# Optimization experiments

Hardware: AMD Instinct MI355X
Metric: run time of the kernel (lower is better)

The kernel has to match this reference:

```python
import jax, jax.numpy as jnp
import numpy as np

K = 16          # num clusters
DZ = 64         # dim_zt == dim_zi (required by decoder matmul)
DT = 1024       # treatment feature dim (dim_t)
NT = 2048       # number of treatments == dim_x (columns of input_ins)
NI = 4096       # number of instances
MU_P_WT = 5.0
COS_EPS = 1e-6


def setup_inputs() -> dict:
    key = jax.random.key(0)
    ks = jax.random.split(key, 12)
    s = 0.02
    return {
        "input_ins": jax.random.uniform(ks[0], (NI, NT), dtype=jnp.float32),
        "input_treat": jax.random.normal(ks[1], (NT, DT), dtype=jnp.float32),
        # nn.Linear params (torch layout: W [out, in], y = x @ W.T + b)
        "W_mu_zt": jax.random.normal(ks[2], (DZ, DT)) * s,
        "b_mu_zt": jnp.zeros((DZ,), jnp.float32),
        "W_lv_zt": jax.random.normal(ks[3], (DZ, DT)) * s,
        "b_lv_zt": jnp.zeros((DZ,), jnp.float32),
        "W_arec": jax.random.normal(ks[4], (DT, DZ)) * s,
        "b_arec": jnp.zeros((DT,), jnp.float32),
        "W_mu_zi": jax.random.normal(ks[5], (DZ, NT)) * s,
        "b_mu_zi": jnp.zeros((DZ,), jnp.float32),
        "W_lv_zi": jax.random.normal(ks[6], (DZ, NT)) * s,
        "b_lv_zi": jnp.zeros((DZ,), jnp.float32),
        "mu_p_zt": jax.random.normal(ks[7], (K, DZ), dtype=jnp.float32),
        "logvar_p_zt": jnp.ones((K, DZ), jnp.float32),
        "W_y1": jax.random.normal(ks[8], (K * DZ, DZ)) * s,
        "b_y1": jnp.zeros((K * DZ,), jnp.float32),
        "W_y2": jax.random.normal(ks[9], (1, K * DZ)) * s,
        "b_y2": jnp.zeros((1,), jnp.float32),
    }


def reference(input_ins, input_treat, W_mu_zt, b_mu_zt, W_lv_zt, b_lv_zt,
              W_arec, b_arec, W_mu_zi, b_mu_zi, W_lv_zi, b_lv_zi,
              mu_p_zt, logvar_p_zt, W_y1, b_y1, W_y2, b_y2):
    # encode_t (eval mode: zt_sample = mu_zt)
    mu_zt = input_treat @ W_mu_zt.T + b_mu_zt           # [NT, DZ]
    logvar_zt = input_treat @ W_lv_zt.T + b_lv_zt       # [NT, DZ]
    zt = mu_zt

    # compute_qc (cosine similarity vs scaled cluster centers, *10)
    centers = MU_P_WT * mu_p_zt                          # [K, DZ]
    num = zt @ centers.T                                 # [NT, K]
    denom = jnp.maximum(
        jnp.linalg.norm(zt, axis=1, keepdims=True) * jnp.linalg.norm(centers, axis=1)[None, :],
        COS_EPS)
    qc_raw = 10.0 * num / denom                          # [NT, K]
    cates = jax.nn.softmax(qc_raw, axis=1)               # forward softmaxes qc once
    c_sample = jax.nn.softmax(cates, axis=1)             # encode_i (eval) softmaxes again

    # encode_i, vectorized over K clusters: (input_ins * cates_k) @ W.T + b
    # fused einsum avoids materializing the [K, NI, NT] masked inputs
    mu_zi = jnp.einsum('nt,tk,dt->knd', input_ins, c_sample, W_mu_zi) + b_mu_zi       # [K, NI, DZ]
    logvar_zi = jnp.einsum('nt,tk,dt->knd', input_ins, c_sample, W_lv_zi) + b_lv_zi   # [K, NI, DZ]
    zi = mu_zi  # eval-mode reparameterize

    # a_reconstby_zt
    a_reconst = jax.nn.sigmoid(zt @ W_arec.T + b_arec)   # [NT, DT]

    # decoder: sum_k sigmoid(zi_k @ zt.T) * cates_k
    logits = jnp.einsum('knd,td->knt', zi, zt)           # [K, NI, NT]
    a_pred = jnp.einsum('knt,tk->nt', jax.nn.sigmoid(logits), c_sample)  # [NI, NT]

    # predictY
    zi_all = jnp.transpose(zi, (1, 0, 2)).reshape(zi.shape[1], K * DZ)   # cat over k, dim=1
    a_zt = input_ins @ zt                                # [NI, DZ]
    rep_w1 = a_zt @ W_y1.T + b_y1                        # [NI, K*DZ]
    pred_y2 = zi_all @ W_y2.T + b_y2                     # [NI, 1]
    # diag(rep_w1 @ zi_all.T) == rowwise dot product (no NIxNI matmul)
    mu_y = jnp.sum(rep_w1 * zi_all, axis=1, keepdims=True) + pred_y2     # [NI, 1]
    logvar_y = jnp.ones_like(mu_y)

    return (mu_zt, logvar_zt, mu_p_zt, logvar_p_zt, cates, mu_zi, logvar_zi,
            zi, a_pred, mu_y, logvar_y, a_reconst)
```

## Files before the change

### kernel.cpp

```cpp
#include <hip/hip_runtime.h>

typedef unsigned short ushort_t;
typedef unsigned int   uint32;
typedef __attribute__((ext_vector_type(8))) short short8;
typedef __attribute__((ext_vector_type(4))) float f32x4;

#define DEV __device__ __forceinline__

#define KC 16
#define DZ 64
#define DT 1024
#define NT 2048
#define NI 4096
#define KD 1024

#define O_MU_ZT   0
#define O_LV_ZT   131072
#define O_MU_P    262144
#define O_LV_P    263168
#define O_CATES   264192
#define O_MU_ZI   296960
#define O_LV_ZI   4491264
#define O_ZI      8685568
#define O_APRED   12879872
#define O_MU_Y    21268480
#define O_LV_Y    21272576
#define O_AREC    21276672

#define WSF_ZT   0
#define WSF_C    131072
#define WSF_CT   163840
#define WSF_AZT  196608
#define WSF_END  458752
#define WSU_ZTB  0
#define WSU_BC   131072
#define WSU_ZIB  4325376
#define WSU_INSB 8519680
#define WSU_ZHT  16908288
#define WSU_ZLT  17039360

DEV ushort_t f2b(float f){
  uint32 u = __float_as_uint(f);
  u += 0x7fffu + ((u >> 16) & 1u);
  return (ushort_t)(u >> 16);
}
DEV uint32 pk(float lo, float hi){
  return (__float_as_uint(hi) & 0xffff0000u) | (__float_as_uint(lo) >> 16);
}
DEV float wred64(float v){
#pragma unroll
  for (int m = 32; m; m >>= 1) v += __shfl_xor(v, m, 64);
  return v;
}
DEV float fastrcp(float x){ return __builtin_amdgcn_rcpf(x); }
DEV void gl2lds16(ushort_t* l, const ushort_t* g){
  __builtin_amdgcn_global_load_lds(
      (const __attribute__((address_space(1))) unsigned int*)g,
      (__attribute__((address_space(3))) unsigned int*)l, 16, 0, 0);
}

__global__ __launch_bounds__(256) void k_encode_t(
    const float* __restrict__ treat, const float* __restrict__ Wmu,
    const float* __restrict__ bmu, const float* __restrict__ Wlv,
    const float* __restrict__ blv, float* __restrict__ out,
    float* __restrict__ ws_zt)
{
  __shared__ float rowsh[8 * DT];
  const int n0 = blockIdx.x * 8, tid = threadIdx.x;
  const float4* src = (const float4*)(treat + (size_t)n0 * DT);
#pragma unroll
  for (int i = 0; i < 8; ++i)
    ((float4*)rowsh)[tid + i * 256] = src[tid + i * 256];
  __syncthreads();
  const int j = tid & 127, half = tid >> 7;
  const bool isMu = j < 64;
  const int jj = j & 63;
  const float* W = (isMu ? Wmu : Wlv) + (size_t)jj * DT;
  const float bias = isMu ? bmu[jj] : blv[jj];
  float a0 = bias, a1 = bias, a2 = bias, a3 = bias;
  const float4* w4 = (const float4*)W;
  const float4* r0 = (const float4*)&rowsh[(half*4 + 0) * DT];
  const float4* r1 = (const float4*)&rowsh[(half*4 + 1) * DT];
  const float4* r2 = (const float4*)&rowsh[(half*4 + 2) * DT];
  const float4* r3 = (const float4*)&rowsh[(half*4 + 3) * DT];
#pragma unroll 4
  for (int i = 0; i < DT / 4; ++i){
    float4 wv = w4[i];
    float4 v0 = r0[i], v1 = r1[i], v2 = r2[i], v3 = r3[i];
    a0 += wv.x*v0.x + wv.y*v0.y + wv.z*v0.z + wv.w*v0.w;
    a1 += wv.x*v1.x + wv.y*v1.y + wv.z*v1.z + wv.w*v1.w;
    a2 += wv.x*v2.x + wv.y*v2.y + wv.z*v2.z + wv.w*v2.w;
    a3 += wv.x*v3.x + wv.y*v3.y + wv.z*v3.z + wv.w*v3.w;
  }
  float acc[4] = {a0, a1, a2, a3};
#pragma unroll
  for (int r = 0; r < 4; ++r){
    const int row = n0 + half*4 + r;
    if (isMu){ out[O_MU_ZT + row*DZ + jj] = acc[r]; ws_zt[row*DZ + jj] = acc[r]; }
    else     { out[O_LV_ZT + row*DZ + jj] = acc[r]; }
  }
}

__global__ __launch_bounds__(256) void k_qc(
    const float* __restrict__ mu_p, const float* __restrict__ ws_zt,
    float* __restrict__ out, float* __restrict__ ws_c, float* __restrict__ ws_cT)
{
  const int tid = threadIdx.x, lane = tid & 63;
  const int row = blockIdx.x * 4 + (tid >> 6);
  const float z = ws_zt[row * DZ + lane];
  const float nz = sqrtf(wred64(z * z));
  float myqc = 0.f;
#pragma unroll
  for (int k = 0; k < KC; ++k){
    float cv  = 5.f * mu_p[k * DZ + lane];
    float dot = wred64(z * cv);
    float nc2 = wred64(cv * cv);
    float qc  = 10.f * dot / fmaxf(nz * sqrtf(nc2), 1e-6f);
    if (lane == k) myqc = qc;
  }
  float mx = myqc;
#pragma unroll
  for (int m = 8; m; m >>= 1) mx = fmaxf(mx, __shfl_xor(mx, m, 16));
  float e = __expf(myqc - mx);
  float s = e;
#pragma unroll
  for (int m = 8; m; m >>= 1) s += __shfl_xor(s, m, 16);
  float cates = e / s;
  float mx2 = cates;
#pragma unroll
  for (int m = 8; m; m >>= 1) mx2 = fmaxf(mx2, __shfl_xor(mx2, m, 16));
  float e2 = __expf(cates - mx2);
  float s2 = e2;
#pragma unroll
  for (int m = 8; m; m >>= 1) s2 += __shfl_xor(s2, m, 16);
  float c2 = e2 / s2;
  if (lane < KC){
    out[O_CATES + row * KC + lane] = cates;
    ws_c[row * KC + lane] = c2;
    ws_cT[lane * NT + row] = c2;
  }
}

__global__ __launch_bounds__(256) void k_prep(
    const float* __restrict__ Wmu, const float* __restrict__ Wlv,
    const float* __restrict__ cT, const float* __restrict__ zt,
    const float* __restrict__ ins,
    ushort_t* __restrict__ Bc, ushort_t* __restrict__ ztb,
    ushort_t* __restrict__ insb,
    ushort_t* __restrict__ zhT, ushort_t* __restrict__ zlT,
    const float* __restrict__ mu_p, const float* __restrict__ lv_p,
    float* __restrict__ out)
{
  const int bx = blockIdx.x, tid = threadIdx.x;
  if (bx < 2048){
    const int j = bx;
    const bool isMu = j < KD;
    const int kk = (j & (KD-1)) >> 6, d = j & 63;
    const float* W = (isMu ? Wmu : Wlv) + (size_t)d * NT;
    const float* c = cT + (size_t)kk * NT;
    const int t = tid * 8;
    float4 w0 = *(const float4*)(W + t), w1 = *(const float4*)(W + t + 4);
    float4 c0 = *(const float4*)(c + t), c1 = *(const float4*)(c + t + 4);
    ushort_t v[8];
    v[0]=f2b(w0.x*c0.x); v[1]=f2b(w0.y*c0.y); v[2]=f2b(w0.z*c0.z); v[3]=f2b(w0.w*c0.w);
    v[4]=f2b(w1.x*c1.x); v[5]=f2b(w1.y*c1.y); v[6]=f2b(w1.z*c1.z); v[7]=f2b(w1.w*c1.w);
    *(uint4*)(Bc + (size_t)j * NT + t) = *(uint4*)v;
  } else if (bx < 2080){
    const int g = (bx - 2048) * 256 + tid;
    const int base = g * 16;
    const float4* src = (const float4*)(zt + base);
    float4 z0 = src[0], z1 = src[1], z2 = src[2], z3 = src[3];
    ushort_t v[16];
    v[0]=f2b(z0.x); v[1]=f2b(z0.y); v[2]=f2b(z0.z); v[3]=f2b(z0.w);
    v[4]=f2b(z1.x); v[5]=f2b(z1.y); v[6]=f2b(z1.z); v[7]=f2b(z1.w);
    v[8]=f2b(z2.x); v[9]=f2b(z2.y); v[10]=f2b(z2.z); v[11]=f2b(z2.w);
    v[12]=f2b(z3.x); v[13]=f2b(z3.y); v[14]=f2b(z3.z); v[15]=f2b(z3.w);
    *(uint4*)(ztb + base) = *(uint4*)&v[0];
    *(uint4*)(ztb + base + 8) = *(uint4*)&v[8];
  } else if (bx < 2084){
    const int i = (bx - 2080) * 256 + tid;
    out[O_MU_P + i] = mu_p[i];
    out[O_LV_P + i] = lv_p[i];
  } else if (bx < 4132){
    const int g = (bx - 2084) * 256 + tid;
    const int base = g * 16;
    const float4* src = (const float4*)(ins + base);
    float4 z0 = src[0], z1 = src[1], z2 = src[2], z3 = src[3];
    ushort_t v[16];
    v[0]=f2b(z0.x); v[1]=f2b(z0.y); v[2]=f2b(z0.z); v[3]=f2b(z0.w);
    v[4]=f2b(z1.x); v[5]=f2b(z1.y); v[6]=f2b(z1.z); v[7]=f2b(z1.w);
    v[8]=f2b(z2.x); v[9]=f2b(z2.y); v[10]=f2b(z2.z); v[11]=f2b(z2.w);
    v[12]=f2b(z3.x); v[13]=f2b(z3.y); v[14]=f2b(z3.z); v[15]=f2b(z3.w);
    *(uint4*)(insb + base) = *(uint4*)&v[0];
    *(uint4*)(insb + base + 8) = *(uint4*)&v[8];
  } else {
    __shared__ float zsh[64 * 65];
    const int t0 = (bx - 4132) * 64;
#pragma unroll
    for (int jj = 0; jj < 16; ++jj){
      const int idx = jj * 256 + tid;
      const int t = idx >> 6, d = idx & 63;
      zsh[t * 65 + d] = zt[(size_t)(t0 + t) * DZ + d];
    }
    __syncthreads();
    const int d = tid >> 2, tq = tid & 3;
    ushort_t vh[16], vl[16];
#pragma unroll
    for (int i = 0; i < 16; ++i){
      const float f = zsh[(tq * 16 + i) * 65 + d];
      const uint32 u = __float_as_uint(f);
      vh[i] = (ushort_t)(u >> 16);
      const float hf = __uint_as_float(u & 0xffff0000u);
      vl[i] = (ushort_t)(__float_as_uint(f - hf) >> 16);
    }
    *(uint4*)(zhT + (size_t)d * NT + t0 + tq * 16)     = *(uint4*)&vh[0];
    *(uint4*)(zhT + (size_t)d * NT + t0 + tq * 16 + 8) = *(uint4*)&vh[8];
    *(uint4*)(zlT + (size_t)d * NT + t0 + tq * 16)     = *(uint4*)&vl[0];
    *(uint4*)(zlT + (size_t)d * NT + t0 + tq * 16 + 8) = *(uint4*)&vl[8];
  }
}

__global__ __launch_bounds__(256) void k_encode_i(
    const ushort_t* __restrict__ insb, const ushort_t* __restrict__ Bc,
    const float* __restrict__ bmu, const float* __restrict__ blv,
    float* __restrict__ out, ushort_t* __restrict__ zib)
{
  __shared__ ushort_t As[2*128*64];
  __shared__ ushort_t Bs[2*128*64];
  const int tid = threadIdx.x;
  const int orig = blockIdx.y * 16 + blockIdx.x;
  const int swz  = (orig & 7) * 64 + (orig >> 3);
  const int j0 = (swz & 15) * 128, n0 = (swz >> 4) * 128;
  const int w = tid >> 6, lane = tid & 63;
  const int wm = w & 1, wn = w >> 1;
  const int l16 = lane & 15, quad = lane >> 4;

  const int srow = tid >> 3, schunk = (tid & 7) ^ (srow & 7);
  const ushort_t* aSrc = insb + (size_t)(n0 + srow) * NT + schunk * 8;
  const ushort_t* bSrc = Bc  + (size_t)(j0 + srow) * NT + schunk * 8;

  f32x4 acc[4][4] = {};

#pragma unroll
  for (int i = 0; i < 4; ++i){
    gl2lds16(&As[tid*8] + i * 2048, aSrc + (size_t)i * 32 * NT);
    gl2lds16(&Bs[tid*8] + i * 2048, bSrc + (size_t)i * 32 * NT);
  }
  __syncthreads();

  int cur = 0;
  for (int kt = 0; kt < NT/64; ++kt){
    if (kt < NT/64 - 1){
      const ushort_t* ak = aSrc + (kt+1) * 64;
      const ushort_t* bk = bSrc + (kt+1) * 64;
      ushort_t* ad = &As[(cur^1)*8192 + tid*8];
      ushort_t* bd = &Bs[(cur^1)*8192 + tid*8];
#pragma unroll
      for (int i = 0; i < 4; ++i){
        gl2lds16(ad + i * 2048, ak + (size_t)i * 32 * NT);
        gl2lds16(bd + i * 2048, bk + (size_t)i * 32 * NT);
      }
    }
    const ushort_t* Ab = &As[cur*8192];
    const ushort_t* Bb = &Bs[cur*8192];
#pragma unroll
    for (int ks = 0; ks < 2; ++ks){
      const int rsw = ((ks*4 + quad) ^ (l16 & 7)) * 8;
      short8 af[4], bf[4];
#pragma unroll
      for (int mf = 0; mf < 4; ++mf)
        af[mf] = *(const short8*)&Ab[(wm*64 + mf*16 + l16)*64 + rsw];
#pragma unroll
      for (int nf = 0; nf < 4; ++nf)
        bf[nf] = *(const short8*)&Bb[(wn*64 + nf*16 + l16)*64 + rsw];
      __builtin_amdgcn_s_setprio(1);
#pragma unroll
      for (int mf = 0; mf < 4; ++mf)
#pragma unroll
        for (int nf = 0; nf < 4; ++nf)
          acc[mf][nf] = __builtin_amdgcn_mfma_f32_16x16x32_bf16(af[mf], bf[nf], acc[mf][nf], 0, 0, 0);
      __builtin_amdgcn_s_setprio(0);
    }
    __syncthreads();
    cur ^= 1;
  }

  const int colW = j0 + wn * 64;
  const bool isMu = colW < KD;
  const int kk = (colW & (KD - 1)) >> 6;
  const float* bias = isMu ? bmu : blv;
  const size_t zbase = (size_t)kk * (NI * DZ);
#pragma unroll
  for (int mf = 0; mf < 4; ++mf){
    const int r = n0 + wm*64 + mf*16 + quad*4;
#pragma unroll
    for (int nf = 0; nf < 4; ++nf){
      const int d = nf*16 + l16;
      const float bv = bias[d];
#pragma unroll
      for (int reg = 0; reg < 4; ++reg){
        float v = acc[mf][nf][reg] + bv;
        size_t idx = zbase + (size_t)(r + reg)*DZ + d;
        if (isMu){
          out[O_MU_ZI + idx] = v;
          out[O_ZI + idx] = v;
          zib[idx] = f2b(v);
        } else {
          out[O_LV_ZI + idx] = v;
        }
      }
    }
  }
}

__global__ __launch_bounds__(256) void k_decoder(
    const ushort_t* __restrict__ ztb, const ushort_t* __restrict__ zib,
    const float* __restrict__ ws_c, float* __restrict__ out)
{
  __shared__ ushort_t Zt[64*64];
  __shared__ ushort_t Zi[128*64];
  __shared__ float ct[64*17];
  const int tid = threadIdx.x;
  const int t0 = blockIdx.x * 64, n0 = blockIdx.y * 128;
  const int w = tid >> 6, lane = tid & 63;
  const int wm = w & 1, wn = w >> 1;
  const int l16 = lane & 15, quad = lane >> 4;
  const int zr = tid >> 2, zq = tid & 3;
  const int ir = tid >> 1, ih = tid & 1;
  {
    const uint4* src = (const uint4*)(ztb + (size_t)(t0 + zr)*DZ + zq*16);
    uint4 z0 = src[0], z1 = src[1];
    ushort_t* dst = &Zt[zr*64];
    *(uint4*)&dst[((zq*2 + 0) ^ (zr & 7)) * 8] = z0;
    *(uint4*)&dst[((zq*2 + 1) ^ (zr & 7)) * 8] = z1;
  }
  for (int i = tid; i < 64*16; i += 256){
    int t = i >> 4, k = i & 15;
    ct[t*17 + k] = ws_c[(size_t)(t0 + t)*KC + k];
  }
  __syncthreads();
  short8 bfh[2][2];
#pragma unroll
  for (int ks = 0; ks < 2; ++ks){
    const int rsw = ((ks*4 + quad) ^ (l16 & 7)) * 8;
#pragma unroll
    for (int nf = 0; nf < 2; ++nf)
      bfh[ks][nf] = *(const short8*)&Zt[(wn*32 + nf*16 + l16)*64 + rsw];
  }
  const ushort_t* iG = zib + (size_t)(n0 + ir)*DZ + ih*32;
  ushort_t* isw = &Zi[ir*64];
  const int sw0 = ((ih*4 + 0) ^ (ir & 7)) * 8;
  const int sw1 = ((ih*4 + 1) ^ (ir & 7)) * 8;
  const int sw2 = ((ih*4 + 2) ^ (ir & 7)) * 8;
  const int sw3 = ((ih*4 + 3) ^ (ir & 7)) * 8;
  uint4 Zr0, Zr1, Zr2, Zr3;
  {
    const uint4* zp = (const uint4*)iG;
    Zr0 = zp[0]; Zr1 = zp[1]; Zr2 = zp[2]; Zr3 = zp[3];
  }
  f32x4 accum[4][2] = {};
  for (int k = 0; k < KC; ++k){
    __syncthreads();
    *(uint4*)&isw[sw0] = Zr0; *(uint4*)&isw[sw1] = Zr1;
    *(uint4*)&isw[sw2] = Zr2; *(uint4*)&isw[sw3] = Zr3;
    __syncthreads();
    if (k < KC - 1){
      const uint4* zp = (const uint4*)(iG + (size_t)(k+1)*(NI*DZ));
      Zr0 = zp[0]; Zr1 = zp[1]; Zr2 = zp[2]; Zr3 = zp[3];
    }
    f32x4 s[4][2] = {};
#pragma unroll
    for (int ks = 0; ks < 2; ++ks){
      const int rsw = ((ks*4 + quad) ^ (l16 & 7)) * 8;
      short8 af[4];
#pragma unroll
      for (int mf = 0; mf < 4; ++mf)
        af[mf] = *(const short8*)&Zi[(wm*64 + mf*16 + l16)*64 + rsw];
#pragma unroll
      for (int mf = 0; mf < 4; ++mf)
#pragma unroll
        for (int nf = 0; nf < 2; ++nf)
          s[mf][nf] = __builtin_amdgcn_mfma_f32_16x16x32_bf16(af[mf], bfh[ks][nf], s[mf][nf], 0, 0, 0);
    }
#pragma unroll
    for (int nf = 0; nf < 2; ++nf){
      const float cv = ct[(wn*32 + nf*16 + l16)*17 + k];
#pragma unroll
      for (int mf = 0; mf < 4; ++mf)
#pragma unroll
        for (int reg = 0; reg < 4; ++reg)
          accum[mf][nf][reg] += cv * fastrcp(1.f + __expf(-s[mf][nf][reg]));
    }
  }
#pragma unroll
  for (int mf = 0; mf < 4; ++mf){
    const int r = n0 + wm*64 + mf*16 + quad*4;
#pragma unroll
    for (int nf = 0; nf < 2; ++nf){
      const int col = t0 + wn*32 + nf*16 + l16;
#pragma unroll
      for (int reg = 0; reg < 4; ++reg)
        out[O_APRED + (size_t)(r + reg)*NT + col] = accum[mf][nf][reg];
    }
  }
}

__global__ __launch_bounds__(512) void k_arec(
    const float* __restrict__ ws_zt, const float* __restrict__ W,
    const float* __restrict__ bias, float* __restrict__ out)
{
  __shared__ float zsh[8 * DZ];
  const int n0 = blockIdx.x * 8, tid = threadIdx.x;
  if (tid < 128)
    ((float4*)zsh)[tid] = ((const float4*)(ws_zt + (size_t)n0 * DZ))[tid];
  __syncthreads();
#pragma unroll
  for (int jo = 0; jo < 2; ++jo){
    const int j = jo*512 + tid;
    const float4* w4 = (const float4*)(W + (size_t)j * DZ);
    const float b = bias[j];
    float acc[8];
#pragma unroll
    for (int r = 0; r < 8; ++r) acc[r] = b;
#pragma unroll
    for (int i = 0; i < 16; ++i){
      float4 wv = w4[i];
#pragma unroll
      for (int r = 0; r < 8; ++r){
        const float* z = &zsh[r*DZ + i*4];
        acc[r] += wv.x*z[0] + wv.y*z[1] + wv.z*z[2] + wv.w*z[3];
      }
    }
#pragma unroll
    for (int r = 0; r < 8; ++r)
      out[O_AREC + (size_t)(n0 + r)*DT + j] = fastrcp(1.f + __expf(-acc[r]));
  }
}

__global__ __launch_bounds__(512) void k_azt(
    const float* __restrict__ ins, const ushort_t* __restrict__ zhT,
    const ushort_t* __restrict__ zlT, float* __restrict__ azt)
{
  __shared__ float red[16*64];
  const int tid = threadIdx.x;
  const int n0 = blockIdx.x * 16;
  const int w = tid >> 6, lane = tid & 63;
  const int kh = w >> 2, wd = w & 3;
  const int l16 = lane & 15, quad = lane >> 4;
  const float* aRow = ins + (size_t)(n0 + l16) * NT + kh * 1024 + quad * 8;
  const ushort_t* bh = zhT + (size_t)(wd * 16 + l16) * NT + kh * 1024 + quad * 8;
  const ushort_t* bl = zlT + (size_t)(wd * 16 + l16) * NT + kh * 1024 + quad * 8;
  f32x4 acc = {};
#pragma unroll 4
  for (int kt = 0; kt < 16; ++kt){
#pragma unroll
    for (int ks = 0; ks < 2; ++ks){
      const int ko = kt * 64 + ks * 32;
      float4 a0 = *(const float4*)(aRow + ko);
      float4 a1 = *(const float4*)(aRow + ko + 4);
      uint32 u0 = __float_as_uint(a0.x), u1 = __float_as_uint(a0.y);
      uint32 u2 = __float_as_uint(a0.z), u3 = __float_as_uint(a0.w);
      uint32 u4 = __float_as_uint(a1.x), u5 = __float_as_uint(a1.y);
      uint32 u6 = __float_as_uint(a1.z), u7 = __float_as_uint(a1.w);
      uint4 H, L;
      H.x = (u1 & 0xffff0000u) | (u0 >> 16);
      H.y = (u3 & 0xffff0000u) | (u2 >> 16);
      H.z = (u5 & 0xffff0000u) | (u4 >> 16);
      H.w = (u7 & 0xffff0000u) | (u6 >> 16);
      float l0 = a0.x - __uint_as_float(u0 & 0xffff0000u);
      float l1 = a0.y - __uint_as_float(u1 & 0xffff0000u);
      float l2 = a0.z - __uint_as_float(u2 & 0xffff0000u);
      float l3 = a0.w - __uint_as_float(u3 & 0xffff0000u);
      float l4 = a1.x - __uint_as_float(u4 & 0xffff0000u);
      float l5 = a1.y - __uint_as_float(u5 & 0xffff0000u);
      float l6 = a1.z - __uint_as_float(u6 & 0xffff0000u);
      float l7 = a1.w - __uint_as_float(u7 & 0xffff0000u);
      L.x = pk(l0, l1); L.y = pk(l2, l3); L.z = pk(l4, l5); L.w = pk(l6, l7);
      short8 ah = *(short8*)&H, al = *(short8*)&L;
      short8 bh8 = *(const short8*)(bh + ko);
      short8 bl8 = *(const short8*)(bl + ko);
      acc = __builtin_amdgcn_mfma_f32_16x16x32_bf16(ah, bh8, acc, 0, 0, 0);
      acc = __builtin_amdgcn_mfma_f32_16x16x32_bf16(al, bh8, acc, 0, 0, 0);
      acc = __builtin_amdgcn_mfma_f32_16x16x32_bf16(ah, bl8, acc, 0, 0, 0);
    }
  }
  const int col = wd * 16 + l16;
  if (kh == 1){
#pragma unroll
    for (int reg = 0; reg < 4; ++reg)
      red[(quad*4 + reg)*64 + col] = acc[reg];
  }
  __syncthreads();
  if (kh == 0){
#pragma unroll
    for (int reg = 0; reg < 4; ++reg)
      azt[(size_t)(n0 + quad*4 + reg) * DZ + col] = acc[reg] + red[(quad*4 + reg)*64 + col];
  }
}

__global__ __launch_bounds__(512) void k_muy(
    const float* __restrict__ azt, const float* __restrict__ Wy1,
    const float* __restrict__ by1, const float* __restrict__ Wy2,
    const float* __restrict__ by2, const float* __restrict__ zi_out,
    float* __restrict__ out)
{
  __shared__ float sazt[16][DZ];
  const int tid = threadIdx.x;
  const int n0 = blockIdx.x * 16;
  for (int i = tid; i < 16*DZ; i += 512)
    sazt[i >> 6][i & 63] = azt[(size_t)(n0 + (i >> 6))*DZ + (i & 63)];
  __syncthreads();
  const int w = tid >> 6, lane = tid & 63;
  float s0 = 0.f, s1 = 0.f;
  for (int jj = 0; jj < 16; ++jj){
    const int j = jj*64 + lane;
    const float4* wr = (const float4*)(Wy1 + (size_t)j * DZ);
    float d0 = 0.f, d1 = 0.f;
    const float* a0 = sazt[w*2 + 0];
    const float* a1 = sazt[w*2 + 1];
#pragma unroll
    for (int i = 0; i < 16; ++i){
      float4 wv = wr[i];
      d0 += wv.x*a0[i*4] + wv.y*a0[i*4+1] + wv.z*a0[i*4+2] + wv.w*a0[i*4+3];
      d1 += wv.x*a1[i*4] + wv.y*a1[i*4+1] + wv.z*a1[i*4+2] + wv.w*a1[i*4+3];
    }
    const float add = by1[j] + Wy2[j];
    const size_t zb = (size_t)jj*(NI*DZ) + lane;
    s0 += (d0 + add) * zi_out[zb + (size_t)(n0 + w*2 + 0)*DZ];
    s1 += (d1 + add) * zi_out[zb + (size_t)(n0 + w*2 + 1)*DZ];
  }
  s0 = wred64(s0); s1 = wred64(s1);
  if (lane == 0){
    const float b = by2[0];
    out[O_MU_Y + n0 + w*2 + 0] = s0 + b;
    out[O_MU_Y + n0 + w*2 + 1] = s1 + b;
  }
  if (tid < 16) out[O_LV_Y + n0 + tid] = 1.0f;
}

extern "C" void kernel_launch(void* const* d_in, const int* in_sizes, int n_in,
                              void* d_out, int out_size, void* d_ws, size_t ws_size,
                              hipStream_t stream)
{
  (void)in_sizes; (void)n_in; (void)out_size; (void)ws_size;
  const float* ins   = (const float*)d_in[0];
  const float* treat = (const float*)d_in[1];
  const float* Wmzt  = (const float*)d_in[2];
  const float* bmzt  = (const float*)d_in[3];
  const float* Wlzt  = (const float*)d_in[4];
  const float* blzt  = (const float*)d_in[5];
  const float* Warec = (const float*)d_in[6];
  const float* barec = (const float*)d_in[7];
  const float* Wmzi  = (const float*)d_in[8];
  const float* bmzi  = (const float*)d_in[9];
  const float* Wlzi  = (const float*)d_in[10];
  const float* blzi  = (const float*)d_in[11];
  const float* mu_p  = (const float*)d_in[12];
  const float* lv_p  = (const float*)d_in[13];
  const float* Wy1   = (const float*)d_in[14];
  const float* by1   = (const float*)d_in[15];
  const float* Wy2   = (const float*)d_in[16];
  const float* by2   = (const float*)d_in[17];
  float* out = (float*)d_out;
  float* wsf = (float*)d_ws;
  ushort_t* wsu = (ushort_t*)(wsf + WSF_END);

  float* ws_zt  = wsf + WSF_ZT;
  float* ws_c   = wsf + WSF_C;
  float* ws_cT  = wsf + WSF_CT;
  float* ws_azt = wsf + WSF_AZT;
  ushort_t* ztb  = wsu + WSU_ZTB;
  ushort_t* Bc   = wsu + WSU_BC;
  ushort_t* zib  = wsu + WSU_ZIB;
  ushort_t* insb = wsu + WSU_INSB;
  ushort_t* zhT  = wsu + WSU_ZHT;
  ushort_t* zlT  = wsu + WSU_ZLT;

  k_encode_t<<<NT/8, 256, 0, stream>>>(treat, Wmzt, bmzt, Wlzt, blzt, out, ws_zt);
  k_qc      <<<NT/4, 256, 0, stream>>>(mu_p, ws_zt, out, ws_c, ws_cT);
  k_prep    <<<4164, 256, 0, stream>>>(Wmzi, Wlzi, ws_cT, ws_zt, ins, Bc, ztb, insb, zhT, zlT, mu_p, lv_p, out);
  k_encode_i<<<dim3(16, 32), 256, 0, stream>>>(insb, Bc, bmzi, blzi, out, zib);
  k_decoder <<<dim3(32, 32), 256, 0, stream>>>(ztb, zib, ws_c, out);
  k_arec    <<<NT/8, 512, 0, stream>>>(ws_zt, Warec, barec, out);
  k_azt     <<<NI/16, 512, 0, stream>>>(ins, zhT, zlT, ws_azt);
  k_muy     <<<NI/16, 512, 0, stream>>>(ws_azt, Wy1, by1, Wy2, by2, out + O_ZI, out);
}
```

Baseline: 426.9 us.

## Replace double-buffered LDS pipeline with single buffer in encode_i GEMM

Removes double buffering in the k_encode_i GEMM. Each k-tile is now loaded into a single LDS buffer, followed by a barrier and then the MFMA work. The s_setprio hints around the MFMA block are also dropped. This halves LDS use per block, which may allow more resident blocks per CU, but it gives up overlapping global-to-LDS loads with compute inside a block.

After: 426.5 us. Within noise of the previous version (-0.1%).

```diff
diff --git a/kernel.cpp b/kernel.cpp
--- a/kernel.cpp
+++ b/kernel.cpp
@@ -225,8 +225,8 @@
     const float* __restrict__ bmu, const float* __restrict__ blv,
     float* __restrict__ out, ushort_t* __restrict__ zib)
 {
-  __shared__ ushort_t As[2*128*64];
-  __shared__ ushort_t Bs[2*128*64];
+  __shared__ ushort_t As[128*64];
+  __shared__ ushort_t Bs[128*64];
   const int tid = threadIdx.x;
   const int orig = blockIdx.y * 16 + blockIdx.x;
   const int swz  = (orig & 7) * 64 + (orig >> 3);
@@ -238,51 +238,37 @@
   const int srow = tid >> 3, schunk = (tid & 7) ^ (srow & 7);
   const ushort_t* aSrc = insb + (size_t)(n0 + srow) * NT + schunk * 8;
   const ushort_t* bSrc = Bc  + (size_t)(j0 + srow) * NT + schunk * 8;
+  ushort_t* aDst = &As[tid * 8];
+  ushort_t* bDst = &Bs[tid * 8];
 
   f32x4 acc[4][4] = {};
 
-#pragma unroll
-  for (int i = 0; i < 4; ++i){
-    gl2lds16(&As[tid*8] + i * 2048, aSrc + (size_t)i * 32 * NT);
-    gl2lds16(&Bs[tid*8] + i * 2048, bSrc + (size_t)i * 32 * NT);
-  }
-  __syncthreads();
-
-  int cur = 0;
   for (int kt = 0; kt < NT/64; ++kt){
-    if (kt < NT/64 - 1){
-      const ushort_t* ak = aSrc + (kt+1) * 64;
-      const ushort_t* bk = bSrc + (kt+1) * 64;
-      ushort_t* ad = &As[(cur^1)*8192 + tid*8];
-      ushort_t* bd = &Bs[(cur^1)*8192 + tid*8];
-#pragma unroll
-      for (int i = 0; i < 4; ++i){
-        gl2lds16(ad + i * 2048, ak + (size_t)i * 32 * NT);
-        gl2lds16(bd + i * 2048, bk + (size_t)i * 32 * NT);
-      }
-    }
-    const ushort_t* Ab = &As[cur*8192];
-    const ushort_t* Bb = &Bs[cur*8192];
+    const ushort_t* ak = aSrc + kt * 64;
+    const ushort_t* bk = bSrc + kt * 64;
+#pragma unroll
+    for (int i = 0; i < 4; ++i){
+      gl2lds16(aDst + i * 2048, ak + (size_t)i * 32 * NT);
+      gl2lds16(bDst + i * 2048, bk + (size_t)i * 32 * NT);
+    }
+    __syncthreads();
 #pragma unroll
     for (int ks = 0; ks < 2; ++ks){
       const int rsw = ((ks*4 + quad) ^ (l16 & 7)) * 8;
       short8 af[4], bf[4];
 #pragma unroll
       for (int mf = 0; mf < 4; ++mf)
-        af[mf] = *(const short8*)&Ab[(wm*64 + mf*16 + l16)*64 + rsw];
+        af[mf] = *(const short8*)&As[(wm*64 + mf*16 + l16)*64 + rsw];
 #pragma unroll
       for (int nf = 0; nf < 4; ++nf)
-        bf[nf] = *(const short8*)&Bb[(wn*64 + nf*16 + l16)*64 + rsw];
-      __builtin_amdgcn_s_setprio(1);
+        bf[nf] = *(const short8*)&Bs[(wn*64 + nf*16 + l16)*64 + rsw];
 #pragma unroll
       for (int mf = 0; mf < 4; ++mf)
 #pragma unroll
         for (int nf = 0; nf < 4; ++nf)
           acc[mf][nf] = __builtin_amdgcn_mfma_f32_16x16x32_bf16(af[mf], bf[nf], acc[mf][nf], 0, 0, 0);
-      __builtin_amdgcn_s_setprio(0);
     }
     __syncthreads();
-    cur ^= 1;
   }
 
   const int colW = j0 + wn * 64;
```
